# Performance work log

Hardware: AMD Instinct MI355X
Metric: run time of the kernel (lower is better)

## Reference

```python
import jax, jax.numpy as jnp
import numpy as np

N_VERT = 163842  # icosphere level-7 vertex count
IN_FEATS = 64
OUT_FEATS = 64
BATCH = 2
K = 7  # center vertex + 6 one-ring neighbors


def setup_inputs() -> dict:
    key = jax.random.key(0)
    k1, k2, k3, k4 = jax.random.split(key, 4)
    x = jax.random.normal(k1, (N_VERT, IN_FEATS, BATCH), dtype=jnp.float32)
    neigh_orders = jax.random.randint(k2, (K * N_VERT,), 0, N_VERT, dtype=jnp.int64)
    W = jax.random.normal(k3, (OUT_FEATS, K * IN_FEATS), dtype=jnp.float32) * 0.05
    b = jax.random.normal(k4, (OUT_FEATS,), dtype=jnp.float32) * 0.05
    return {"x": x, "neigh_orders": neigh_orders, "W": W, "b": b}


def reference(x, neigh_orders, W, b):
    # x: [N, C, B]; neigh_orders: [7N] flat indices, grouped per-vertex (n*7 + k)
    N = x.shape[0]
    C = x.shape[1]
    idx = neigh_orders.reshape(N, K)            # [N, 7]
    gathered = x[idx]                           # [N, 7, C, B] irregular gather
    Wr = W.reshape(W.shape[0], K, C)            # [O, 7, C] matches flatten order (k*C + c)
    # out[n, o, b] = sum_{k,c} gathered[n,k,c,b] * W[o, k*C + c] + b[o]
    out = jnp.einsum("nkcb,okc->nob", gathered, Wr) + b[None, :, None]
    return out  # [N, O, B]
```

## Files before the change

### kernel.cpp

```cpp
#include <hip/hip_runtime.h>

#define NV      163842
#define CIN     64
#define KN      7
#define NKMAX   (NV * KN)
#define KDIM    448
#define KSTEPS  14
#define VPC     16
#define ROWS    32
#define ASTRIDE 456

typedef short  short8 __attribute__((ext_vector_type(8)));
typedef float  f32x4  __attribute__((ext_vector_type(4)));

static __device__ __forceinline__ unsigned int pack_bf16(float a, float b) {
#if __has_builtin(__builtin_amdgcn_cvt_pk_bf16_f32)
    typedef __bf16 bf16x2 __attribute__((ext_vector_type(2)));
    union { bf16x2 v; unsigned int u; } cv;
    cv.v = __builtin_amdgcn_cvt_pk_bf16_f32(a, b);
    return cv.u;
#else
    unsigned int ua = __float_as_uint(a);
    unsigned int ub = __float_as_uint(b);
    ua = (ua + 0x7FFFu + ((ua >> 16) & 1u)) >> 16;
    ub = (ub + 0x7FFFu + ((ub >> 16) & 1u)) & 0xFFFF0000u;
    return ua | ub;
#endif
}

static __device__ __forceinline__ void bar_lgkm() {
    asm volatile("s_waitcnt lgkmcnt(0)\n\ts_barrier" ::: "memory");
}

__global__ __launch_bounds__(256)
void xcast(const float* __restrict__ x, unsigned int* __restrict__ xt, int nf4)
{
    const int f = blockIdx.x * 256 + threadIdx.x;
    if (f >= nf4) return;
    const f32x4 g = __builtin_nontemporal_load(&((const f32x4*)x)[f]);
    const int v = f >> 5;
    const int r = f & 31;
    xt[v * 64 + r]      = pack_bf16(g[0], g[2]);
    xt[v * 64 + 32 + r] = pack_bf16(g[1], g[3]);
}

__global__ __launch_bounds__(256, 3)
void onering_mfma_bf16_v4(const unsigned short* __restrict__ xt,
                          const int* __restrict__ neigh,
                          const float* __restrict__ W,
                          const float* __restrict__ bias,
                          float* __restrict__ out,
                          int nchunks)
{
    __shared__ unsigned short A_lds[ROWS * ASTRIDE];
    __shared__ float          C_lds[VPC * 128];

    const int tid  = threadIdx.x;
    const int lane = tid & 63;
    const int w    = tid >> 6;
    const int ncol = lane & 15;
    const int kgrp = lane >> 4;
    const int G    = gridDim.x;

    short8 bfrag[KSTEPS];
    {
        const int o = w * 16 + ncol;
#pragma unroll
        for (int s = 0; s < KSTEPS; ++s) {
            const int kb = s * 32 + kgrp * 8;
            const float4* wp = (const float4*)(W + o * KDIM + kb);
            float4 w0 = wp[0];
            float4 w1 = wp[1];
            union { short8 v; unsigned int u[4]; } pk;
            pk.u[0] = pack_bf16(w0.x, w0.y);
            pk.u[1] = pack_bf16(w0.z, w0.w);
            pk.u[2] = pack_bf16(w1.x, w1.y);
            pk.u[3] = pack_bf16(w1.z, w1.w);
            bfrag[s] = pk.v;
        }
    }
    const float biasv = bias[w * 16 + ncol];

    const int l8 = tid & 7;
    int nidx[7];
    int lbyte[7];
    int soff[7];
#pragma unroll
    for (int i = 0; i < 7; ++i) {
        const int seg = (tid >> 3) + 32 * i;
        const int lv  = seg / 14;
        const int rem = seg - lv * 14;
        const int k   = rem >> 1;
        const int bb  = rem & 1;
        nidx[i]  = lv * KN + k;
        lbyte[i] = (2 * lv + bb) * (ASTRIDE * 2) + k * 128 + l8 * 16;
        soff[i]  = bb * 64 + l8 * 8;
    }

    const int ch0 = blockIdx.x;
    int    I[7];
    short8 R[7];

#pragma unroll
    for (int i = 0; i < 7; ++i) {
        int gi = ch0 * (VPC * KN) + nidx[i];
        I[i] = __builtin_nontemporal_load(&neigh[gi < NKMAX ? gi : 0]);
    }
#pragma unroll
    for (int i = 0; i < 7; ++i)
        R[i] = *(const short8*)(xt + (size_t)I[i] * 128 + soff[i]);
#pragma unroll
    for (int i = 0; i < 7; ++i) {
        int gi = (ch0 + G) * (VPC * KN) + nidx[i];
        I[i] = __builtin_nontemporal_load(&neigh[gi < NKMAX ? gi : 0]);
    }

    for (int ch = ch0; ch < nchunks; ch += G) {
        const int vb = ch * VPC;

        bar_lgkm();

#pragma unroll
        for (int i = 0; i < 7; ++i)
            *(short8*)((char*)A_lds + lbyte[i]) = R[i];
#pragma unroll
        for (int i = 0; i < 7; ++i)
            R[i] = *(const short8*)(xt + (size_t)I[i] * 128 + soff[i]);
#pragma unroll
        for (int i = 0; i < 7; ++i) {
            int gi = (ch + 2 * G) * (VPC * KN) + nidx[i];
            I[i] = __builtin_nontemporal_load(&neigh[gi < NKMAX ? gi : 0]);
        }

        bar_lgkm();

        f32x4 acc0 = {0.f, 0.f, 0.f, 0.f};
        f32x4 acc1 = {0.f, 0.f, 0.f, 0.f};
#pragma unroll
        for (int s = 0; s < KSTEPS; ++s) {
            const int kb = s * 32 + kgrp * 8;
            const short8 a0 = *(const short8*)&A_lds[ncol * ASTRIDE + kb];
            const short8 a1 = *(const short8*)&A_lds[(16 + ncol) * ASTRIDE + kb];
            acc0 = __builtin_amdgcn_mfma_f32_16x16x32_bf16(a0, bfrag[s], acc0, 0, 0, 0);
            acc1 = __builtin_amdgcn_mfma_f32_16x16x32_bf16(a1, bfrag[s], acc1, 0, 0, 0);
        }

        const int o2 = (w * 16 + ncol) * 2;
#pragma unroll
        for (int j = 0; j < 4; ++j) {
            const int r  = kgrp * 4 + j;
            C_lds[(r >> 1) * 128 + o2 + (r & 1)] = acc0[j] + biasv;
            const int r2 = 16 + r;
            C_lds[(r2 >> 1) * 128 + o2 + (r2 & 1)] = acc1[j] + biasv;
        }

        bar_lgkm();

        f32x4* dst = (f32x4*)(out + vb * 128);
#pragma unroll
        for (int it = 0; it < 2; ++it) {
            const int fidx = tid + 256 * it;
            if (vb + (fidx >> 5) < NV)
                __builtin_nontemporal_store(((const f32x4*)C_lds)[fidx], &dst[fidx]);
        }
    }
}

__global__ __launch_bounds__(256, 4)
void onering_mfma_f32(const float* __restrict__ x,
                      const int* __restrict__ neigh,
                      const float* __restrict__ W,
                      const float* __restrict__ bias,
                      float* __restrict__ out,
                      int nchunks)
{
    __shared__ unsigned short A_lds[ROWS * ASTRIDE];
    const int tid  = threadIdx.x;
    const int lane = tid & 63;
    const int w    = tid >> 6;
    const int ncol = lane & 15;
    const int kgrp = lane >> 4;

    short8 bfrag[KSTEPS];
    {
        const int o = w * 16 + ncol;
#pragma unroll
        for (int s = 0; s < KSTEPS; ++s) {
            const int kb = s * 32 + kgrp * 8;
            const float4* wp = (const float4*)(W + o * KDIM + kb);
            float4 w0 = wp[0];
            float4 w1 = wp[1];
            union { short8 v; unsigned int u[4]; } pk;
            pk.u[0] = pack_bf16(w0.x, w0.y);
            pk.u[1] = pack_bf16(w0.z, w0.w);
            pk.u[2] = pack_bf16(w1.x, w1.y);
            pk.u[3] = pack_bf16(w1.z, w1.w);
            bfrag[s] = pk.v;
        }
    }
    const float biasv = bias[w * 16 + ncol];
    const int off4  = tid & 31;
    const int sbase = tid >> 5;

    for (int ch = blockIdx.x; ch < nchunks; ch += gridDim.x) {
        const int vb = ch * VPC;
        __syncthreads();
#pragma unroll
        for (int i = 0; i < 14; ++i) {
            const int s  = sbase + 8 * i;
            const int lv = s / 7;
            const int k  = s - lv * 7;
            const int n  = vb + lv;
            int vi = 0;
            if (n < NV) vi = neigh[n * KN + k];
            const float4 g = ((const float4*)x)[vi * 32 + off4];
            const int base = k * 64 + 2 * off4;
            ((unsigned int*)A_lds)[((lv * 2)     * ASTRIDE + base) >> 1] = pack_bf16(g.x, g.z);
            ((unsigned int*)A_lds)[((lv * 2 + 1) * ASTRIDE + base) >> 1] = pack_bf16(g.y, g.w);
        }
        __syncthreads();
        f32x4 acc0 = {0.f, 0.f, 0.f, 0.f};
        f32x4 acc1 = {0.f, 0.f, 0.f, 0.f};
#pragma unroll
        for (int s = 0; s < KSTEPS; ++s) {
            const int kb = s * 32 + kgrp * 8;
            const short8 a0 = *(const short8*)&A_lds[ncol * ASTRIDE + kb];
            const short8 a1 = *(const short8*)&A_lds[(16 + ncol) * ASTRIDE + kb];
            acc0 = __builtin_amdgcn_mfma_f32_16x16x32_bf16(a0, bfrag[s], acc0, 0, 0, 0);
            acc1 = __builtin_amdgcn_mfma_f32_16x16x32_bf16(a1, bfrag[s], acc1, 0, 0, 0);
        }
        const int o = w * 16 + ncol;
#pragma unroll
        for (int j = 0; j < 4; ++j) {
            const int r = kgrp * 4 + j;
            {
                const int lv = r >> 1, bb = r & 1, n = vb + lv;
                if (n < NV) out[n * 128 + o * 2 + bb] = acc0[j] + biasv;
            }
            {
                const int m = 16 + r;
                const int lv = m >> 1, bb = m & 1, n = vb + lv;
                if (n < NV) out[n * 128 + o * 2 + bb] = acc1[j] + biasv;
            }
        }
    }
}

extern "C" void kernel_launch(void* const* d_in, const int* in_sizes, int n_in,
                              void* d_out, int out_size, void* d_ws, size_t ws_size,
                              hipStream_t stream) {
    const float* x     = (const float*)d_in[0];
    const int*   neigh = (const int*)d_in[1];
    const float* W     = (const float*)d_in[2];
    const float* bias  = (const float*)d_in[3];
    float*       out   = (float*)d_out;

    const int nchunks = (NV + VPC - 1) / VPC;
    const size_t need = (size_t)NV * 128 * sizeof(unsigned short);

    if (ws_size >= need) {
        unsigned short* xt = (unsigned short*)d_ws;
        const int nf4 = NV * 32;
        xcast<<<dim3((nf4 + 255) / 256), dim3(256), 0, stream>>>(x, (unsigned int*)xt, nf4);
        onering_mfma_bf16_v4<<<dim3(1024), dim3(256), 0, stream>>>(xt, neigh, W, bias, out, nchunks);
    } else {
        onering_mfma_f32<<<dim3(2560), dim3(256), 0, stream>>>(x, neigh, W, bias, out, nchunks);
    }
}
```

Before: 209.7 us.

## Gather neighbor rows via direct global-to-LDS DMA with double-buffered swizzled LDS

The gathered bf16 neighbor rows now go straight into LDS through global_load_lds 16-byte DMA, replacing the register round trip. The A tile is double-buffered and uses an XOR-swizzled segment layout, and neighbor indices are prefetched one extra chunk ahead. The aim is to drop VGPR staging and the separate LDS store, and to overlap the next chunk's gather with the current MFMA work. In exchange, occupancy falls to 2 blocks per CU with the grid halved to 512, LDS use doubles, and the hand-placed vmcnt waits must match the compiler's load ordering exactly.

After: 204.2 us. 2.6% less time.

```diff
diff --git a/kernel.cpp b/kernel.cpp
--- a/kernel.cpp
+++ b/kernel.cpp
@@ -8,6 +8,8 @@
 #define KSTEPS  14
 #define VPC     16
 #define ROWS    32
+#define NSEG    224
+#define ABUFS   (NSEG * 64)
 #define ASTRIDE 456
 
 typedef short  short8 __attribute__((ext_vector_type(8)));
@@ -32,6 +34,14 @@
     asm volatile("s_waitcnt lgkmcnt(0)\n\ts_barrier" ::: "memory");
 }
 
+#define WAITVM(N) asm volatile("s_waitcnt vmcnt(" #N ")" ::: "memory")
+
+static __device__ __forceinline__ void dma16(const unsigned short* g, unsigned short* l) {
+    __builtin_amdgcn_global_load_lds(
+        (const __attribute__((address_space(1))) unsigned int*)g,
+        (__attribute__((address_space(3))) unsigned int*)l, 16, 0, 0);
+}
+
 __global__ __launch_bounds__(256)
 void xcast(const float* __restrict__ x, unsigned int* __restrict__ xt, int nf4)
 {
@@ -44,16 +54,16 @@
     xt[v * 64 + 32 + r] = pack_bf16(g[1], g[3]);
 }
 
-__global__ __launch_bounds__(256, 3)
-void onering_mfma_bf16_v4(const unsigned short* __restrict__ xt,
+__global__ __launch_bounds__(256, 2)
+void onering_mfma_bf16_v5(const unsigned short* __restrict__ xt,
                           const int* __restrict__ neigh,
                           const float* __restrict__ W,
                           const float* __restrict__ bias,
                           float* __restrict__ out,
                           int nchunks)
 {
-    __shared__ unsigned short A_lds[ROWS * ASTRIDE];
-    __shared__ float          C_lds[VPC * 128];
+    __shared__ __align__(16) unsigned short A_lds[2 * ABUFS];
+    __shared__ __align__(16) float          C_lds[VPC * 128];
 
     const int tid  = threadIdx.x;
     const int lane = tid & 63;
@@ -83,8 +93,8 @@
 
     const int l8 = tid & 7;
     int nidx[7];
-    int lbyte[7];
-    int soff[7];
+    int ldst[7];
+    int gso[7];
 #pragma unroll
     for (int i = 0; i < 7; ++i) {
         const int seg = (tid >> 3) + 32 * i;
@@ -92,55 +102,70 @@
         const int rem = seg - lv * 14;
         const int k   = rem >> 1;
         const int bb  = rem & 1;
-        nidx[i]  = lv * KN + k;
-        lbyte[i] = (2 * lv + bb) * (ASTRIDE * 2) + k * 128 + l8 * 16;
-        soff[i]  = bb * 64 + l8 * 8;
+        nidx[i] = lv * KN + k;
+        ldst[i] = seg * 64 + l8 * 8;
+        gso[i]  = bb * 64 + ((l8 ^ (seg & 7)) << 3);
     }
 
     const int ch0 = blockIdx.x;
-    int    I[7];
-    short8 R[7];
+    int I[7];
+    int I2[7];
 
 #pragma unroll
     for (int i = 0; i < 7; ++i) {
         int gi = ch0 * (VPC * KN) + nidx[i];
         I[i] = __builtin_nontemporal_load(&neigh[gi < NKMAX ? gi : 0]);
     }
+    WAITVM(0);
 #pragma unroll
     for (int i = 0; i < 7; ++i)
-        R[i] = *(const short8*)(xt + (size_t)I[i] * 128 + soff[i]);
+        dma16(xt + (size_t)I[i] * 128 + gso[i], A_lds + ldst[i]);
 #pragma unroll
     for (int i = 0; i < 7; ++i) {
         int gi = (ch0 + G) * (VPC * KN) + nidx[i];
-        I[i] = __builtin_nontemporal_load(&neigh[gi < NKMAX ? gi : 0]);
-    }
-
+        I2[i] = __builtin_nontemporal_load(&neigh[gi < NKMAX ? gi : 0]);
+    }
+    WAITVM(0);
+#pragma unroll
+    for (int i = 0; i < 7; ++i) I[i] = I2[i];
+#pragma unroll
+    for (int i = 0; i < 7; ++i) {
+        int gi = (ch0 + 2 * G) * (VPC * KN) + nidx[i];
+        I2[i] = __builtin_nontemporal_load(&neigh[gi < NKMAX ? gi : 0]);
+    }
+
+    int cur = 0;
     for (int ch = ch0; ch < nchunks; ch += G) {
         const int vb = ch * VPC;
 
-        bar_lgkm();
-
+        unsigned short* Aw = A_lds + (cur ^ 1) * ABUFS;
 #pragma unroll
         for (int i = 0; i < 7; ++i)
-            *(short8*)((char*)A_lds + lbyte[i]) = R[i];
-#pragma unroll
-        for (int i = 0; i < 7; ++i)
-            R[i] = *(const short8*)(xt + (size_t)I[i] * 128 + soff[i]);
+            dma16(xt + (size_t)I[i] * 128 + gso[i], Aw + ldst[i]);
+
+        WAITVM(14);
+        __builtin_amdgcn_s_barrier();
+
+        WAITVM(7);
+#pragma unroll
+        for (int i = 0; i < 7; ++i) I[i] = I2[i];
 #pragma unroll
         for (int i = 0; i < 7; ++i) {
-            int gi = (ch + 2 * G) * (VPC * KN) + nidx[i];
-            I[i] = __builtin_nontemporal_load(&neigh[gi < NKMAX ? gi : 0]);
-        }
-
-        bar_lgkm();
-
+            int gi = (ch + 3 * G) * (VPC * KN) + nidx[i];
+            I2[i] = __builtin_nontemporal_load(&neigh[gi < NKMAX ? gi : 0]);
+        }
+
+        const unsigned short* Ab = A_lds + cur * ABUFS;
+        const int rb0 = (ncol >> 1) * 14 + (ncol & 1);
         f32x4 acc0 = {0.f, 0.f, 0.f, 0.f};
         f32x4 acc1 = {0.f, 0.f, 0.f, 0.f};
 #pragma unroll
         for (int s = 0; s < KSTEPS; ++s) {
-            const int kb = s * 32 + kgrp * 8;
-            const short8 a0 = *(const short8*)&A_lds[ncol * ASTRIDE + kb];
-            const short8 a1 = *(const short8*)&A_lds[(16 + ncol) * ASTRIDE + kb];
+            const int p0   = (s & 1) * 4 + kgrp;
+            const int seg0 = rb0 + (s >> 1) * 2;
+            const int slot = (p0 ^ (seg0 & 7)) << 3;
+            const short8 a0 = *(const short8*)&Ab[seg0 * 64 + slot];
+            const short8 a1 = *(const short8*)&Ab[(seg0 + 112) * 64 + slot];
             acc0 = __builtin_amdgcn_mfma_f32_16x16x32_bf16(a0, bfrag[s], acc0, 0, 0, 0);
             acc1 = __builtin_amdgcn_mfma_f32_16x16x32_bf16(a1, bfrag[s], acc1, 0, 0, 0);
         }
@@ -153,9 +178,7 @@
             const int r2 = 16 + r;
             C_lds[(r2 >> 1) * 128 + o2 + (r2 & 1)] = acc1[j] + biasv;
         }
-
         bar_lgkm();
-
         f32x4* dst = (f32x4*)(out + vb * 128);
 #pragma unroll
         for (int it = 0; it < 2; ++it) {
@@ -163,6 +186,8 @@
             if (vb + (fidx >> 5) < NV)
                 __builtin_nontemporal_store(((const f32x4*)C_lds)[fidx], &dst[fidx]);
         }
+
+        cur ^= 1;
     }
 }
 
@@ -262,7 +287,7 @@
         unsigned short* xt = (unsigned short*)d_ws;
         const int nf4 = NV * 32;
         xcast<<<dim3((nf4 + 255) / 256), dim3(256), 0, stream>>>(x, (unsigned int*)xt, nf4);
-        onering_mfma_bf16_v4<<<dim3(1024), dim3(256), 0, stream>>>(xt, neigh, W, bias, out, nchunks);
+        onering_mfma_bf16_v5<<<dim3(512), dim3(256), 0, stream>>>(xt, neigh, W, bias, out, nchunks);
     } else {
         onering_mfma_f32<<<dim3(2560), dim3(256), 0, stream>>>(x, neigh, W, bias, out, nchunks);
     }
```
